# Kernel optimization log

Measured on AMD Instinct MI355X. Metric: run time of the kernel, lower is better.

Reference implementation:

```python
import jax, jax.numpy as jnp
import numpy as np

E = 16      # num_experts
K = 4       # num_experts_per_tok
H = 2048    # hidden_size
I = 1408    # moe_intermediate_size
SI = 5632   # shared expert intermediate size
CAP = 1024
NORM_TOPK = False


def setup_inputs() -> dict:
    key = jax.random.key(0)
    ks = jax.random.split(key, 9)
    def w(k, shape, fan_in):
        return jax.random.normal(k, shape, jnp.float32) * (fan_in ** -0.5)
    return {
        "hidden_states": jax.random.normal(ks[0], (1, 2048, H), jnp.float32),
        "gate_w":  w(ks[1], (E, H), H),        # router: Linear(H -> E), no bias
        "we_gate": w(ks[2], (E, I, H), H),     # per-expert gate_proj weights
        "we_up":   w(ks[3], (E, I, H), H),     # per-expert up_proj weights
        "we_down": w(ks[4], (E, H, I), I),     # per-expert down_proj weights
        "ws_gate": w(ks[5], (SI, H), H),       # shared expert gate_proj
        "ws_up":   w(ks[6], (SI, H), H),       # shared expert up_proj
        "ws_down": w(ks[7], (H, SI), SI),      # shared expert down_proj
        "sg_w":    w(ks[8], (1, H), H),        # shared_expert_gate: Linear(H -> 1)
    }


def reference(hidden_states, gate_w, we_gate, we_up, we_down,
              ws_gate, ws_up, ws_down, sg_w):
    B, S, Hd = hidden_states.shape
    x = hidden_states.reshape(-1, Hd)                      # [T, H]
    T = x.shape[0]

    # --- router ---
    router_logits = x @ gate_w.T                           # [T, E]
    probs = jax.nn.softmax(router_logits.astype(jnp.float32), axis=-1)
    topw, topi = jax.lax.top_k(probs, K)                   # [T, K]
    if NORM_TOPK:
        topw = topw / topw.sum(axis=-1, keepdims=True)

    # --- dispatch: flatten (token, slot) assignments ---
    A = T * K
    fe = topi.reshape(A)                                   # expert id per assignment
    fw = topw.reshape(A)                                   # routing weight per assignment
    ft = jnp.repeat(jnp.arange(T), K)                      # token id per assignment
    # position of each assignment within its expert (rank in arrival order)
    oh = jax.nn.one_hot(fe, E, dtype=jnp.int32)            # [A, E]
    pos = jnp.take_along_axis(jnp.cumsum(oh, axis=0) - 1, fe[:, None], axis=1)[:, 0]
    valid = pos < CAP
    # scatter tokens into per-expert buffers; overflow goes to dummy row CAP
    buf = jnp.zeros((E, CAP + 1, Hd), x.dtype)
    buf = buf.at[fe, jnp.where(valid, pos, CAP)].set(x[ft])[:, :CAP]  # [E, C, H]

    # --- per-expert SiLU-gated MLP (batched grouped GEMMs) ---
    g = jnp.einsum('ech,eih->eci', buf, we_gate)
    u = jnp.einsum('ech,eih->eci', buf, we_up)
    eo = jnp.einsum('eci,ehi->ech', jax.nn.silu(g) * u, we_down)      # [E, C, H]

    # --- combine: weighted scatter-add back to tokens ---
    ga = eo[fe, jnp.minimum(pos, CAP - 1)]                 # [A, H]
    wcomb = (fw * valid.astype(fw.dtype)).astype(x.dtype)
    y = jnp.zeros((T, Hd), x.dtype).at[ft].add(ga * wcomb[:, None])

    # --- shared expert with sigmoid gate ---
    sh = (jax.nn.silu(x @ ws_gate.T) * (x @ ws_up.T)) @ ws_down.T
    sh = jax.nn.sigmoid(x @ sg_w.T) * sh

    out = (y + sh).reshape(B, S, Hd)
    return out, router_logits
```

## Files before the change

### kernel.cpp

```cpp
#include <hip/hip_runtime.h>

#define T_TOK 2048
#define NE 16
#define KTOP 4
#define HD 2048
#define ID 1408
#define SID 5632
#define CAPACITY 1024

typedef __attribute__((ext_vector_type(8))) short short8;
typedef __attribute__((ext_vector_type(4))) float floatx4;

__device__ __forceinline__ short f2b(float f){
  union { float f; unsigned u; } v; v.f = f;
  unsigned r = v.u + 0x7fffu + ((v.u >> 16) & 1u);
  return (short)(r >> 16);
}
__device__ __forceinline__ float b2f(short s){
  union { float f; unsigned u; } v; v.u = ((unsigned)(unsigned short)s) << 16;
  return v.f;
}
__device__ __forceinline__ void gl16(const void* g, void* l){
  __builtin_amdgcn_global_load_lds(
      (const __attribute__((address_space(1))) void*)g,
      (__attribute__((address_space(3))) void*)l, 16, 0, 0);
}

__global__ void moe_zero(int* __restrict__ counts){
  if (threadIdx.x < NE) counts[threadIdx.x] = 0;
}

__global__ void moe_convert_all(const float* __restrict__ eg, const float* __restrict__ eu,
                                const float* __restrict__ ed, const float* __restrict__ sgp,
                                const float* __restrict__ sup, const float* __restrict__ sdp,
                                short* __restrict__ dst)
{
  const long long EW = (long long)NE * ID * HD / 8;
  const long long SW = (long long)SID * HD / 8;
  const long long total = 3 * EW + 3 * SW;
  long long stride = (long long)gridDim.x * blockDim.x;
  for (long long i = (long long)blockIdx.x * blockDim.x + threadIdx.x; i < total; i += stride){
    const float* s; long long j;
    if (i < 2 * EW){
      if (i < EW){ s = eg; j = i; } else { s = eu; j = i - EW; }
    } else if (i < 3 * EW){ s = ed; j = i - 2 * EW; }
    else if (i < 3 * EW + SW){ s = sgp; j = i - 3 * EW; }
    else if (i < 3 * EW + 2 * SW){ s = sup; j = i - 3 * EW - SW; }
    else { s = sdp; j = i - 3 * EW - 2 * SW; }
    float4 f0 = ((const float4*)s)[j * 2];
    float4 f1 = ((const float4*)s)[j * 2 + 1];
    short8 v = { f2b(f0.x), f2b(f0.y), f2b(f0.z), f2b(f0.w),
                 f2b(f1.x), f2b(f1.y), f2b(f1.z), f2b(f1.w) };
    ((short8*)dst)[i] = v;
  }
}

__global__ void moe_router(const float* __restrict__ x,
                           const float* __restrict__ gate_w,
                           const float* __restrict__ sg_w,
                           float* __restrict__ logits_out,
                           short* __restrict__ xb,
                           int* __restrict__ counts,
                           int* __restrict__ slot_token,
                           float* __restrict__ slot_w,
                           int* __restrict__ tslot,
                           float* __restrict__ tw,
                           float* __restrict__ sg)
{
  int wave = threadIdx.x >> 6, lane = threadIdx.x & 63;
  int t = (blockIdx.x << 2) + wave;
  if (t >= T_TOK) return;
  const float4* xr = (const float4*)(x + (size_t)t * HD);
  short8* xbw = (short8*)(xb + (size_t)t * HD);
  float acc[17];
  #pragma unroll
  for (int e = 0; e < 17; ++e) acc[e] = 0.f;
  #pragma unroll
  for (int j = 0; j < 4; ++j){
    int i4 = (j * 64 + lane) * 2;
    float4 x0 = xr[i4], x1 = xr[i4 + 1];
    short8 v = { f2b(x0.x), f2b(x0.y), f2b(x0.z), f2b(x0.w),
                 f2b(x1.x), f2b(x1.y), f2b(x1.z), f2b(x1.w) };
    xbw[j * 64 + lane] = v;
    #pragma unroll
    for (int e = 0; e < 16; ++e){
      const float4* gr = (const float4*)(gate_w + e * HD);
      float4 g0 = gr[i4], g1 = gr[i4 + 1];
      acc[e] += x0.x*g0.x + x0.y*g0.y + x0.z*g0.z + x0.w*g0.w
              + x1.x*g1.x + x1.y*g1.y + x1.z*g1.z + x1.w*g1.w;
    }
    const float4* sr = (const float4*)sg_w;
    float4 s0 = sr[i4], s1 = sr[i4 + 1];
    acc[16] += x0.x*s0.x + x0.y*s0.y + x0.z*s0.z + x0.w*s0.w
             + x1.x*s1.x + x1.y*s1.y + x1.z*s1.z + x1.w*s1.w;
  }
  #pragma unroll
  for (int e = 0; e < 17; ++e){
    float v = acc[e];
    #pragma unroll
    for (int off = 32; off > 0; off >>= 1) v += __shfl_xor(v, off, 64);
    acc[e] = v;
  }
  if (lane == 0){
    float m = acc[0];
    #pragma unroll
    for (int e = 1; e < 16; ++e) m = fmaxf(m, acc[e]);
    float p[16]; float s = 0.f;
    #pragma unroll
    for (int e = 0; e < 16; ++e){ p[e] = expf(acc[e] - m); s += p[e]; }
    float inv = 1.f / s;
    #pragma unroll
    for (int e = 0; e < 16; ++e) logits_out[t * 16 + e] = acc[e];
    unsigned used = 0;
    for (int k = 0; k < KTOP; ++k){
      float best = -1.f; int bi = 0;
      #pragma unroll
      for (int e = 0; e < 16; ++e){
        float pe = ((used >> e) & 1u) ? -1.f : p[e];
        if (pe > best){ best = pe; bi = e; }
      }
      used |= (1u << bi);
      int pos = atomicAdd(&counts[bi], 1);
      int enc = -1;
      if (pos < CAPACITY){
        slot_token[bi * CAPACITY + pos] = t;
        slot_w[bi * CAPACITY + pos] = best * inv;
        enc = bi * CAPACITY + pos;
      }
      tslot[t * KTOP + k] = enc;
      tw[t * KTOP + k] = best * inv;
    }
    sg[t] = 1.f / (1.f + expf(-acc[16]));
  }
}


template<int BF16W>
__global__ __launch_bounds__(256) void moe_gateup(
    const short* __restrict__ Asrc,
    const void* __restrict__ Wg_, const void* __restrict__ Wu_,
    short* __restrict__ Out,
    const int* __restrict__ counts, const int* __restrict__ slot_token,
    int Ndim, int Kdim, int expert_mode, int mtiles, int ntiles)
{
  int nwg = gridDim.x;
  int wg = ((blockIdx.x & 7) * (nwg >> 3)) + (blockIdx.x >> 3);
  int m_t = wg % mtiles; wg /= mtiles;
  int n_t = wg % ntiles; int e = wg / ntiles;

  int cnt = T_TOK; size_t woff = 0; short* out = Out;
  if (expert_mode){
    cnt = counts[e]; if (cnt > CAPACITY) cnt = CAPACITY;
    if (m_t * 128 >= cnt) return;
    woff = (size_t)e * Ndim * Kdim;
    out = Out + (size_t)e * CAPACITY * Ndim;
  }
  const int m0 = m_t * 128, n0 = n_t * 64;

  __shared__ __align__(16) char smem[2][32768];

  const int tid = threadIdx.x;
  const int lane = tid & 63, wave = tid >> 6;
  const int wr = wave >> 1, wc = wave & 1;
  const int lrow = lane & 15, lk = lane >> 4;

  const int srow = tid >> 3, pslot = tid & 7;
  const int lslot = pslot ^ (srow & 7);

  const short* aptr[4];
  #pragma unroll
  for (int i = 0; i < 4; ++i){
    int p = m0 + i * 32 + srow;
    const short* base;
    if (expert_mode){
      int q = (p < cnt) ? p : 0;
      base = Asrc + (size_t)slot_token[e * CAPACITY + q] * Kdim;
    } else base = Asrc + (size_t)p * Kdim;
    aptr[i] = base + (lslot << 3);
  }
  const short *bgp[2], *bup[2];
  const float *bgf[2], *buf2[2];
  #pragma unroll
  for (int i = 0; i < 2; ++i){
    size_t roff = (size_t)(n0 + i * 32 + srow) * Kdim + (lslot << 3);
    if (BF16W){
      bgp[i] = (const short*)Wg_ + woff + roff;
      bup[i] = (const short*)Wu_ + woff + roff;
    } else {
      bgf[i]  = (const float*)Wg_ + woff + roff;
      buf2[i] = (const float*)Wu_ + woff + roff;
    }
  }

  const floatx4 vzero = {0.f, 0.f, 0.f, 0.f};
  floatx4 accg[4][2], accu[4][2];
  #pragma unroll
  for (int i = 0; i < 4; ++i)
    #pragma unroll
    for (int j = 0; j < 2; ++j){ accg[i][j] = vzero; accu[i][j] = vzero; }

  const int fxor = lrow & 7;
  const int arowb = (wr * 64 + lrow) << 7;
  const int browb = (wc * 32 + lrow) << 7;

  if (BF16W){
    {
      char* b = smem[0];
      #pragma unroll
      for (int i = 0; i < 4; ++i) gl16(aptr[i], b + i * 4096 + tid * 16);
      #pragma unroll
      for (int i = 0; i < 2; ++i) gl16(bgp[i], b + 16384 + i * 4096 + tid * 16);
      #pragma unroll
      for (int i = 0; i < 2; ++i) gl16(bup[i], b + 24576 + i * 4096 + tid * 16);
    }
    __syncthreads();
    int cur = 0;
    for (int k0 = 0; k0 < Kdim; k0 += 64){
      if (k0 + 64 < Kdim){
        char* b = smem[cur ^ 1];
        #pragma unroll
        for (int i = 0; i < 4; ++i) gl16(aptr[i] + k0 + 64, b + i * 4096 + tid * 16);
        #pragma unroll
        for (int i = 0; i < 2; ++i) gl16(bgp[i] + k0 + 64, b + 16384 + i * 4096 + tid * 16);
        #pragma unroll
        for (int i = 0; i < 2; ++i) gl16(bup[i] + k0 + 64, b + 24576 + i * 4096 + tid * 16);
      }
      const char* bb = smem[cur];
      #pragma unroll
      for (int kh = 0; kh < 2; ++kh){
        const int soff = (((kh << 2) | lk) ^ fxor) << 4;
        short8 a[4], bg[2], bu[2];
        #pragma unroll
        for (int mf = 0; mf < 4; ++mf)
          a[mf] = *(const short8*)(bb + arowb + (mf << 11) + soff);
        #pragma unroll
        for (int nf = 0; nf < 2; ++nf){
          bg[nf] = *(const short8*)(bb + 16384 + browb + (nf << 11) + soff);
          bu[nf] = *(const short8*)(bb + 24576 + browb + (nf << 11) + soff);
        }
        #pragma unroll
        for (int mf = 0; mf < 4; ++mf)
          #pragma unroll
          for (int nf = 0; nf < 2; ++nf){
            accg[mf][nf] = __builtin_amdgcn_mfma_f32_16x16x32_bf16(a[mf], bg[nf], accg[mf][nf], 0, 0, 0);
            accu[mf][nf] = __builtin_amdgcn_mfma_f32_16x16x32_bf16(a[mf], bu[nf], accu[mf][nf], 0, 0, 0);
          }
      }
      __syncthreads();
      cur ^= 1;
    }
  } else {
    char* sA = smem[0]; char* sBg = sA + 16384; char* sBu = sA + 24576;
    for (int k0 = 0; k0 < Kdim; k0 += 64){
      __syncthreads();
      #pragma unroll
      for (int i = 0; i < 4; ++i){
        short8 v = *(const short8*)(aptr[i] + k0);
        *(short8*)(sA + i * 4096 + tid * 16) = v;
      }
      #pragma unroll
      for (int i = 0; i < 2; ++i){
        float4 f0 = *(const float4*)(bgf[i] + k0);
        float4 f1 = *(const float4*)(bgf[i] + k0 + 4);
        short8 v = { f2b(f0.x), f2b(f0.y), f2b(f0.z), f2b(f0.w),
                     f2b(f1.x), f2b(f1.y), f2b(f1.z), f2b(f1.w) };
        *(short8*)(sBg + i * 4096 + tid * 16) = v;
        float4 g0 = *(const float4*)(buf2[i] + k0);
        float4 g1 = *(const float4*)(buf2[i] + k0 + 4);
        short8 w = { f2b(g0.x), f2b(g0.y), f2b(g0.z), f2b(g0.w),
                     f2b(g1.x), f2b(g1.y), f2b(g1.z), f2b(g1.w) };
        *(short8*)(sBu + i * 4096 + tid * 16) = w;
      }
      __syncthreads();
      #pragma unroll
      for (int kh = 0; kh < 2; ++kh){
        const int soff = (((kh << 2) | lk) ^ fxor) << 4;
        short8 a[4], bg[2], bu[2];
        #pragma unroll
        for (int mf = 0; mf < 4; ++mf)
          a[mf] = *(const short8*)(sA + arowb + (mf << 11) + soff);
        #pragma unroll
        for (int nf = 0; nf < 2; ++nf){
          bg[nf] = *(const short8*)(sBg + browb + (nf << 11) + soff);
          bu[nf] = *(const short8*)(sBu + browb + (nf << 11) + soff);
        }
        #pragma unroll
        for (int mf = 0; mf < 4; ++mf)
          #pragma unroll
          for (int nf = 0; nf < 2; ++nf){
            accg[mf][nf] = __builtin_amdgcn_mfma_f32_16x16x32_bf16(a[mf], bg[nf], accg[mf][nf], 0, 0, 0);
            accu[mf][nf] = __builtin_amdgcn_mfma_f32_16x16x32_bf16(a[mf], bu[nf], accu[mf][nf], 0, 0, 0);
          }
      }
    }
  }

  const int colbase = n0 + wc * 32 + lrow;
  #pragma unroll
  for (int mf = 0; mf < 4; ++mf){
    int pr = m0 + wr * 64 + mf * 16 + lk * 4;
    #pragma unroll
    for (int nf = 0; nf < 2; ++nf){
      floatx4 g4 = accg[mf][nf], u4 = accu[mf][nf];
      int col = colbase + nf * 16;
      #pragma unroll
      for (int r = 0; r < 4; ++r){
        float gv = g4[r], uv = u4[r];
        float a = (gv / (1.f + __expf(-gv))) * uv;
        out[(size_t)(pr + r) * Ndim + col] = f2b(a);
      }
    }
  }
}

template<int BF16W, int NF>
__global__ __launch_bounds__(256) void moe_down(
    const short* __restrict__ Asrc, const void* __restrict__ Wd_,
    float* __restrict__ y, short* __restrict__ eo,
    const int* __restrict__ counts, const int* __restrict__ slot_token,
    const float* __restrict__ slot_w, const float* __restrict__ sgate,
    int Kdim, int expert_mode, int mtiles, int ntiles)
{
  constexpr int BN = NF * 32;
  int nwg = gridDim.x;
  int wg = ((blockIdx.x & 7) * (nwg >> 3)) + (blockIdx.x >> 3);
  int m_t = wg % mtiles; wg /= mtiles;
  int n_t = wg % ntiles; int e = wg / ntiles;

  int cnt = T_TOK; const short* ab = Asrc; size_t woff = 0;
  if (expert_mode){
    cnt = counts[e]; if (cnt > CAPACITY) cnt = CAPACITY;
    if (m_t * 128 >= cnt) return;
    ab = Asrc + (size_t)e * CAPACITY * Kdim;
    woff = (size_t)e * HD * Kdim;
  }
  const int m0 = m_t * 128, n0 = n_t * BN;

  __shared__ __align__(16) char smem[2][16384 + NF * 4096];

  const int tid = threadIdx.x;
  const int lane = tid & 63, wave = tid >> 6;
  const int wr = wave >> 1, wc = wave & 1;
  const int lrow = lane & 15, lk = lane >> 4;

  const int srow = tid >> 3, pslot = tid & 7;
  const int lslot = pslot ^ (srow & 7);

  const short* aptr[4];
  #pragma unroll
  for (int i = 0; i < 4; ++i)
    aptr[i] = ab + (size_t)(m0 + i * 32 + srow) * Kdim + (lslot << 3);
  const short* bbp[NF];
  const float* bbf[NF];
  #pragma unroll
  for (int i = 0; i < NF; ++i){
    size_t roff = (size_t)(n0 + i * 32 + srow) * Kdim + (lslot << 3);
    if (BF16W) bbp[i] = (const short*)Wd_ + woff + roff;
    else       bbf[i] = (const float*)Wd_ + woff + roff;
  }

  const floatx4 vzero = {0.f, 0.f, 0.f, 0.f};
  floatx4 acc[4][NF];
  #pragma unroll
  for (int i = 0; i < 4; ++i)
    #pragma unroll
    for (int j = 0; j < NF; ++j) acc[i][j] = vzero;

  const int fxor = lrow & 7;
  const int arowb = (wr * 64 + lrow) << 7;
  const int browb = (wc * (NF * 16) + lrow) << 7;

  if (BF16W){
    {
      char* b = smem[0];
      #pragma unroll
      for (int i = 0; i < 4; ++i) gl16(aptr[i], b + i * 4096 + tid * 16);
      #pragma unroll
      for (int i = 0; i < NF; ++i) gl16(bbp[i], b + 16384 + i * 4096 + tid * 16);
    }
    __syncthreads();
    int cur = 0;
    for (int k0 = 0; k0 < Kdim; k0 += 64){
      if (k0 + 64 < Kdim){
        char* b = smem[cur ^ 1];
        #pragma unroll
        for (int i = 0; i < 4; ++i) gl16(aptr[i] + k0 + 64, b + i * 4096 + tid * 16);
        #pragma unroll
        for (int i = 0; i < NF; ++i) gl16(bbp[i] + k0 + 64, b + 16384 + i * 4096 + tid * 16);
      }
      const char* bb = smem[cur];
      #pragma unroll
      for (int kh = 0; kh < 2; ++kh){
        const int soff = (((kh << 2) | lk) ^ fxor) << 4;
        short8 a[4], b[NF];
        #pragma unroll
        for (int mf = 0; mf < 4; ++mf)
          a[mf] = *(const short8*)(bb + arowb + (mf << 11) + soff);
        #pragma unroll
        for (int nf = 0; nf < NF; ++nf)
          b[nf] = *(const short8*)(bb + 16384 + browb + (nf << 11) + soff);
        #pragma unroll
        for (int mf = 0; mf < 4; ++mf)
          #pragma unroll
          for (int nf = 0; nf < NF; ++nf)
            acc[mf][nf] = __builtin_amdgcn_mfma_f32_16x16x32_bf16(a[mf], b[nf], acc[mf][nf], 0, 0, 0);
      }
      __syncthreads();
      cur ^= 1;
    }
  } else {
    char* sA = smem[0]; char* sB = sA + 16384;
    for (int k0 = 0; k0 < Kdim; k0 += 64){
      __syncthreads();
      #pragma unroll
      for (int i = 0; i < 4; ++i){
        short8 v = *(const short8*)(aptr[i] + k0);
        *(short8*)(sA + i * 4096 + tid * 16) = v;
      }
      #pragma unroll
      for (int i = 0; i < NF; ++i){
        float4 f0 = *(const float4*)(bbf[i] + k0);
        float4 f1 = *(const float4*)(bbf[i] + k0 + 4);
        short8 w = { f2b(f0.x), f2b(f0.y), f2b(f0.z), f2b(f0.w),
                     f2b(f1.x), f2b(f1.y), f2b(f1.z), f2b(f1.w) };
        *(short8*)(sB + i * 4096 + tid * 16) = w;
      }
      __syncthreads();
      #pragma unroll
      for (int kh = 0; kh < 2; ++kh){
        const int soff = (((kh << 2) | lk) ^ fxor) << 4;
        short8 a[4], b[NF];
        #pragma unroll
        for (int mf = 0; mf < 4; ++mf)
          a[mf] = *(const short8*)(sA + arowb + (mf << 11) + soff);
        #pragma unroll
        for (int nf = 0; nf < NF; ++nf)
          b[nf] = *(const short8*)(sB + browb + (nf << 11) + soff);
        #pragma unroll
        for (int mf = 0; mf < 4; ++mf)
          #pragma unroll
          for (int nf = 0; nf < NF; ++nf)
            acc[mf][nf] = __builtin_amdgcn_mfma_f32_16x16x32_bf16(a[mf], b[nf], acc[mf][nf], 0, 0, 0);
      }
    }
  }

  const int colb = n0 + wc * (NF * 16) + lrow;
  if (expert_mode){
    if (eo){
      #pragma unroll
      for (int mf = 0; mf < 4; ++mf){
        int pr = m0 + wr * 64 + mf * 16 + lk * 4;
        #pragma unroll
        for (int r = 0; r < 4; ++r){
          int p = pr + r;
          #pragma unroll
          for (int nf = 0; nf < NF; ++nf)
            eo[(size_t)(e * CAPACITY + p) * HD + colb + nf * 16] = f2b(acc[mf][nf][r]);
        }
      }
    } else {
      #pragma unroll
      for (int mf = 0; mf < 4; ++mf){
        int pr = m0 + wr * 64 + mf * 16 + lk * 4;
        #pragma unroll
        for (int r = 0; r < 4; ++r){
          int p = pr + r;
          if (p < cnt){
            int tok = slot_token[e * CAPACITY + p];
            float w = slot_w[e * CAPACITY + p];
            #pragma unroll
            for (int nf = 0; nf < NF; ++nf)
              atomicAdd(&y[(size_t)tok * HD + colb + nf * 16], w * acc[mf][nf][r]);
          }
        }
      }
    }
  } else {
    #pragma unroll
    for (int mf = 0; mf < 4; ++mf){
      int pr = m0 + wr * 64 + mf * 16 + lk * 4;
      #pragma unroll
      for (int r = 0; r < 4; ++r){
        int t = pr + r;
        float sv = sgate[t];
        #pragma unroll
        for (int nf = 0; nf < NF; ++nf)
          y[(size_t)t * HD + colb + nf * 16] = sv * acc[mf][nf][r];
      }
    }
  }
}

__global__ void moe_combine(const short* __restrict__ eo,
                            const int* __restrict__ tslot,
                            const float* __restrict__ tw,
                            float* __restrict__ y)
{
  int t = blockIdx.x;
  int o = threadIdx.x << 3;
  float* yp = y + (size_t)t * HD + o;
  float4 a0 = *(const float4*)yp, a1 = *(const float4*)(yp + 4);
  float acc[8] = {a0.x, a0.y, a0.z, a0.w, a1.x, a1.y, a1.z, a1.w};
  #pragma unroll
  for (int k = 0; k < KTOP; ++k){
    int s = tslot[t * KTOP + k];
    if (s >= 0){
      float w = tw[t * KTOP + k];
      short8 v = *(const short8*)(eo + (size_t)s * HD + o);
      #pragma unroll
      for (int j = 0; j < 8; ++j) acc[j] += w * b2f(v[j]);
    }
  }
  float4 r0 = {acc[0], acc[1], acc[2], acc[3]};
  float4 r1 = {acc[4], acc[5], acc[6], acc[7]};
  *(float4*)yp = r0; *(float4*)(yp + 4) = r1;
}

extern "C" void kernel_launch(void* const* d_in, const int* in_sizes, int n_in,
                              void* d_out, int out_size, void* d_ws, size_t ws_size,
                              hipStream_t stream)
{
  (void)in_sizes; (void)n_in; (void)out_size;
  const float* x       = (const float*)d_in[0];
  const float* gate_w  = (const float*)d_in[1];
  const float* we_gate = (const float*)d_in[2];
  const float* we_up   = (const float*)d_in[3];
  const float* we_down = (const float*)d_in[4];
  const float* wsg     = (const float*)d_in[5];
  const float* wsu     = (const float*)d_in[6];
  const float* wsd     = (const float*)d_in[7];
  const float* sg_w    = (const float*)d_in[8];

  float* y      = (float*)d_out;
  float* logits = y + (size_t)T_TOK * HD;

  const size_t SZ_XB  = (size_t)T_TOK * HD * 2;
  const size_t SZ_WE  = (size_t)NE * ID * HD * 2;
  const size_t SZ_WS  = (size_t)SID * HD * 2;
  const size_t SZ_ACT = (size_t)NE * CAPACITY * ID * 2;
  const size_t SZ_ACS = (size_t)T_TOK * SID * 2;
  const size_t SZ_EO  = (size_t)NE * CAPACITY * HD * 2;
  const size_t SZ_SMALL = 65536 + 65536 + 32768 + 32768 + 256 + 8192;

  const size_t NEED_B = SZ_XB + 3 * SZ_WE + 3 * SZ_WS + SZ_ACT + SZ_ACS + SZ_SMALL;
  const size_t NEED_A = NEED_B + SZ_EO;

  char* ws = (char*)d_ws;
  size_t off = 0;
  short* xb   = (short*)(ws + off); off += SZ_XB;
  short* wbeg = (short*)(ws + off); off += SZ_WE;
  short* wbeu = (short*)(ws + off); off += SZ_WE;
  short* wbed = (short*)(ws + off); off += SZ_WE;
  short* wbsg = (short*)(ws + off); off += SZ_WS;
  short* wbsu = (short*)(ws + off); off += SZ_WS;
  short* wbsd = (short*)(ws + off); off += SZ_WS;
  short* act  = (short*)(ws + off); off += SZ_ACT;
  short* acts = (short*)(ws + off); off += SZ_ACS;
  short* eo   = (short*)(ws + off);
  if (ws_size >= NEED_A) off += SZ_EO; else eo = nullptr;
  int*   slot_token = (int*)  (ws + off); off += 65536;
  float* slot_w     = (float*)(ws + off); off += 65536;
  int*   tslot      = (int*)  (ws + off); off += 32768;
  float* tw         = (float*)(ws + off); off += 32768;
  int*   counts     = (int*)  (ws + off); off += 256;
  float* sg         = (float*)(ws + off);

  if (ws_size >= NEED_B){
    moe_zero<<<1, 64, 0, stream>>>(counts);
    moe_convert_all<<<2048, 256, 0, stream>>>(we_gate, we_up, we_down, wsg, wsu, wsd, wbeg);
    moe_router<<<512, 256, 0, stream>>>(x, gate_w, sg_w, logits, xb,
                                        counts, slot_token, slot_w, tslot, tw, sg);
    moe_gateup<1><<<16 * 88, 256, 0, stream>>>(xb, wbsg, wbsu, acts,
                                               nullptr, nullptr, SID, HD, 0, 16, 88);
    moe_gateup<1><<<8 * 22 * NE, 256, 0, stream>>>(xb, wbeg, wbeu, act,
                                                   counts, slot_token, ID, HD, 1, 8, 22);
    moe_down<1, 2><<<16 * 32, 256, 0, stream>>>(acts, wbsd, y, nullptr, nullptr, nullptr,
                                                nullptr, sg, SID, 0, 16, 32);
    moe_down<1, 4><<<8 * 16 * NE, 256, 0, stream>>>(act, wbed, y, eo, counts, slot_token,
                                                    slot_w, nullptr, ID, 1, 8, 16);
    if (eo) moe_combine<<<T_TOK, 256, 0, stream>>>(eo, tslot, tw, y);
  } else {
    size_t o2 = 0;
    short* xb2   = (short*)(ws + o2); o2 += SZ_XB;
    short* act2  = (short*)(ws + o2); o2 += SZ_ACT;
    short* acts2 = (short*)(ws + o2); o2 += SZ_ACS;
    int*   st2 = (int*)  (ws + o2); o2 += 65536;
    float* sw2 = (float*)(ws + o2); o2 += 65536;
    int*   ts2 = (int*)  (ws + o2); o2 += 32768;
    float* tw2 = (float*)(ws + o2); o2 += 32768;
    int*   cn2 = (int*)  (ws + o2); o2 += 256;
    float* sg2 = (float*)(ws + o2);
    moe_zero<<<1, 64, 0, stream>>>(cn2);
    moe_router<<<512, 256, 0, stream>>>(x, gate_w, sg_w, logits, xb2,
                                        cn2, st2, sw2, ts2, tw2, sg2);
    moe_gateup<0><<<16 * 88, 256, 0, stream>>>(xb2, wsg, wsu, acts2,
                                               nullptr, nullptr, SID, HD, 0, 16, 88);
    moe_gateup<0><<<8 * 22 * NE, 256, 0, stream>>>(xb2, we_gate, we_up, act2,
                                                   cn2, st2, ID, HD, 1, 8, 22);
    moe_down<0, 2><<<16 * 32, 256, 0, stream>>>(acts2, wsd, y, nullptr, nullptr, nullptr,
                                                nullptr, sg2, SID, 0, 16, 32);
    moe_down<0, 4><<<8 * 16 * NE, 256, 0, stream>>>(act2, we_down, y, nullptr, cn2, st2,
                                                    sw2, nullptr, ID, 1, 8, 16);
  }
}
```

Before: 841.6 us.

## Fuse fp32-to-bf16 weight conversion into GEMM loaders and drop pre-convert pass

Removes the separate kernel that converted all expert and shared weights to bf16 every call. The grouped GEMMs now read fp32 weights directly into registers, convert them with packed v_cvt_pk_bf16_f32, and write them to the next LDS buffer while the MFMAs consume the current one. The activation tiles keep their async global-to-LDS prefetch. This avoids writing and rereading a full bf16 copy of the weights, but each GEMM now streams twice the weight bytes and spends extra VALU work and registers on conversion. It also changes rounding for tie and NaN cases through the hardware convert instruction.

```diff
diff --git a/kernel.cpp b/kernel.cpp
--- a/kernel.cpp
+++ b/kernel.cpp
@@ -20,6 +20,17 @@
   union { float f; unsigned u; } v; v.u = ((unsigned)(unsigned short)s) << 16;
   return v.f;
 }
+__device__ __forceinline__ unsigned cvt_pk(float a, float b){
+  unsigned r;
+  asm("v_cvt_pk_bf16_f32 %0, %1, %2" : "=v"(r) : "v"(a), "v"(b));
+  return r;
+}
+__device__ __forceinline__ short8 cvt8(float4 a, float4 b){
+  union { unsigned d[4]; short8 s; } u;
+  u.d[0] = cvt_pk(a.x, a.y); u.d[1] = cvt_pk(a.z, a.w);
+  u.d[2] = cvt_pk(b.x, b.y); u.d[3] = cvt_pk(b.z, b.w);
+  return u.s;
+}
 __device__ __forceinline__ void gl16(const void* g, void* l){
   __builtin_amdgcn_global_load_lds(
       (const __attribute__((address_space(1))) void*)g,
@@ -28,31 +39,6 @@
 
 __global__ void moe_zero(int* __restrict__ counts){
   if (threadIdx.x < NE) counts[threadIdx.x] = 0;
-}
-
-__global__ void moe_convert_all(const float* __restrict__ eg, const float* __restrict__ eu,
-                                const float* __restrict__ ed, const float* __restrict__ sgp,
-                                const float* __restrict__ sup, const float* __restrict__ sdp,
-                                short* __restrict__ dst)
-{
-  const long long EW = (long long)NE * ID * HD / 8;
-  const long long SW = (long long)SID * HD / 8;
-  const long long total = 3 * EW + 3 * SW;
-  long long stride = (long long)gridDim.x * blockDim.x;
-  for (long long i = (long long)blockIdx.x * blockDim.x + threadIdx.x; i < total; i += stride){
-    const float* s; long long j;
-    if (i < 2 * EW){
-      if (i < EW){ s = eg; j = i; } else { s = eu; j = i - EW; }
-    } else if (i < 3 * EW){ s = ed; j = i - 2 * EW; }
-    else if (i < 3 * EW + SW){ s = sgp; j = i - 3 * EW; }
-    else if (i < 3 * EW + 2 * SW){ s = sup; j = i - 3 * EW - SW; }
-    else { s = sdp; j = i - 3 * EW - 2 * SW; }
-    float4 f0 = ((const float4*)s)[j * 2];
-    float4 f1 = ((const float4*)s)[j * 2 + 1];
-    short8 v = { f2b(f0.x), f2b(f0.y), f2b(f0.z), f2b(f0.w),
-                 f2b(f1.x), f2b(f1.y), f2b(f1.z), f2b(f1.w) };
-    ((short8*)dst)[i] = v;
-  }
 }
 
 __global__ void moe_router(const float* __restrict__ x,
@@ -79,9 +65,7 @@
   for (int j = 0; j < 4; ++j){
     int i4 = (j * 64 + lane) * 2;
     float4 x0 = xr[i4], x1 = xr[i4 + 1];
-    short8 v = { f2b(x0.x), f2b(x0.y), f2b(x0.z), f2b(x0.w),
-                 f2b(x1.x), f2b(x1.y), f2b(x1.z), f2b(x1.w) };
-    xbw[j * 64 + lane] = v;
+    xbw[j * 64 + lane] = cvt8(x0, x1);
     #pragma unroll
     for (int e = 0; e < 16; ++e){
       const float4* gr = (const float4*)(gate_w + e * HD);
@@ -135,10 +119,9 @@
 }
 
 
-template<int BF16W>
 __global__ __launch_bounds__(256) void moe_gateup(
     const short* __restrict__ Asrc,
-    const void* __restrict__ Wg_, const void* __restrict__ Wu_,
+    const float* __restrict__ Wg_, const float* __restrict__ Wu_,
     short* __restrict__ Out,
     const int* __restrict__ counts, const int* __restrict__ slot_token,
     int Ndim, int Kdim, int expert_mode, int mtiles, int ntiles)
@@ -178,18 +161,12 @@
     } else base = Asrc + (size_t)p * Kdim;
     aptr[i] = base + (lslot << 3);
   }
-  const short *bgp[2], *bup[2];
-  const float *bgf[2], *buf2[2];
+  const float *bsrc[4];
   #pragma unroll
   for (int i = 0; i < 2; ++i){
     size_t roff = (size_t)(n0 + i * 32 + srow) * Kdim + (lslot << 3);
-    if (BF16W){
-      bgp[i] = (const short*)Wg_ + woff + roff;
-      bup[i] = (const short*)Wu_ + woff + roff;
-    } else {
-      bgf[i]  = (const float*)Wg_ + woff + roff;
-      buf2[i] = (const float*)Wu_ + woff + roff;
-    }
+    bsrc[i]     = Wg_ + woff + roff;
+    bsrc[i + 2] = Wu_ + woff + roff;
   }
 
   const floatx4 vzero = {0.f, 0.f, 0.f, 0.f};
@@ -202,97 +179,61 @@
   const int fxor = lrow & 7;
   const int arowb = (wr * 64 + lrow) << 7;
   const int browb = (wc * 32 + lrow) << 7;
-
-  if (BF16W){
-    {
-      char* b = smem[0];
-      #pragma unroll
-      for (int i = 0; i < 4; ++i) gl16(aptr[i], b + i * 4096 + tid * 16);
-      #pragma unroll
-      for (int i = 0; i < 2; ++i) gl16(bgp[i], b + 16384 + i * 4096 + tid * 16);
-      #pragma unroll
-      for (int i = 0; i < 2; ++i) gl16(bup[i], b + 24576 + i * 4096 + tid * 16);
-    }
-    __syncthreads();
-    int cur = 0;
-    for (int k0 = 0; k0 < Kdim; k0 += 64){
-      if (k0 + 64 < Kdim){
-        char* b = smem[cur ^ 1];
-        #pragma unroll
-        for (int i = 0; i < 4; ++i) gl16(aptr[i] + k0 + 64, b + i * 4096 + tid * 16);
-        #pragma unroll
-        for (int i = 0; i < 2; ++i) gl16(bgp[i] + k0 + 64, b + 16384 + i * 4096 + tid * 16);
-        #pragma unroll
-        for (int i = 0; i < 2; ++i) gl16(bup[i] + k0 + 64, b + 24576 + i * 4096 + tid * 16);
-      }
-      const char* bb = smem[cur];
-      #pragma unroll
-      for (int kh = 0; kh < 2; ++kh){
-        const int soff = (((kh << 2) | lk) ^ fxor) << 4;
-        short8 a[4], bg[2], bu[2];
-        #pragma unroll
-        for (int mf = 0; mf < 4; ++mf)
-          a[mf] = *(const short8*)(bb + arowb + (mf << 11) + soff);
+  const int bwoff = 16384 + (tid << 4);
+
+  float4 breg[4][2];
+  #pragma unroll
+  for (int i = 0; i < 4; ++i) gl16(aptr[i], smem[0] + i * 4096 + tid * 16);
+  #pragma unroll
+  for (int i = 0; i < 4; ++i){
+    breg[i][0] = *(const float4*)(bsrc[i]);
+    breg[i][1] = *(const float4*)(bsrc[i] + 4);
+  }
+  #pragma unroll
+  for (int i = 0; i < 4; ++i)
+    *(short8*)(smem[0] + bwoff + i * 4096) = cvt8(breg[i][0], breg[i][1]);
+  __syncthreads();
+
+  int cur = 0;
+  for (int k0 = 0; k0 < Kdim; k0 += 64){
+    const bool more = (k0 + 64) < Kdim;
+    if (more){
+      #pragma unroll
+      for (int i = 0; i < 4; ++i) gl16(aptr[i] + k0 + 64, smem[cur ^ 1] + i * 4096 + tid * 16);
+      #pragma unroll
+      for (int i = 0; i < 4; ++i){
+        breg[i][0] = *(const float4*)(bsrc[i] + k0 + 64);
+        breg[i][1] = *(const float4*)(bsrc[i] + k0 + 68);
+      }
+    }
+    const char* bb = smem[cur];
+    #pragma unroll
+    for (int kh = 0; kh < 2; ++kh){
+      const int soff = (((kh << 2) | lk) ^ fxor) << 4;
+      short8 a[4], bg[2], bu[2];
+      #pragma unroll
+      for (int mf = 0; mf < 4; ++mf)
+        a[mf] = *(const short8*)(bb + arowb + (mf << 11) + soff);
+      #pragma unroll
+      for (int nf = 0; nf < 2; ++nf){
+        bg[nf] = *(const short8*)(bb + 16384 + browb + (nf << 11) + soff);
+        bu[nf] = *(const short8*)(bb + 24576 + browb + (nf << 11) + soff);
+      }
+      #pragma unroll
+      for (int mf = 0; mf < 4; ++mf)
         #pragma unroll
         for (int nf = 0; nf < 2; ++nf){
-          bg[nf] = *(const short8*)(bb + 16384 + browb + (nf << 11) + soff);
-          bu[nf] = *(const short8*)(bb + 24576 + browb + (nf << 11) + soff);
+          accg[mf][nf] = __builtin_amdgcn_mfma_f32_16x16x32_bf16(a[mf], bg[nf], accg[mf][nf], 0, 0, 0);
+          accu[mf][nf] = __builtin_amdgcn_mfma_f32_16x16x32_bf16(a[mf], bu[nf], accu[mf][nf], 0, 0, 0);
         }
-        #pragma unroll
-        for (int mf = 0; mf < 4; ++mf)
-          #pragma unroll
-          for (int nf = 0; nf < 2; ++nf){
-            accg[mf][nf] = __builtin_amdgcn_mfma_f32_16x16x32_bf16(a[mf], bg[nf], accg[mf][nf], 0, 0, 0);
-            accu[mf][nf] = __builtin_amdgcn_mfma_f32_16x16x32_bf16(a[mf], bu[nf], accu[mf][nf], 0, 0, 0);
-          }
-      }
-      __syncthreads();
-      cur ^= 1;
-    }
-  } else {
-    char* sA = smem[0]; char* sBg = sA + 16384; char* sBu = sA + 24576;
-    for (int k0 = 0; k0 < Kdim; k0 += 64){
-      __syncthreads();
-      #pragma unroll
-      for (int i = 0; i < 4; ++i){
-        short8 v = *(const short8*)(aptr[i] + k0);
-        *(short8*)(sA + i * 4096 + tid * 16) = v;
-      }
-      #pragma unroll
-      for (int i = 0; i < 2; ++i){
-        float4 f0 = *(const float4*)(bgf[i] + k0);
-        float4 f1 = *(const float4*)(bgf[i] + k0 + 4);
-        short8 v = { f2b(f0.x), f2b(f0.y), f2b(f0.z), f2b(f0.w),
-                     f2b(f1.x), f2b(f1.y), f2b(f1.z), f2b(f1.w) };
-        *(short8*)(sBg + i * 4096 + tid * 16) = v;
-        float4 g0 = *(const float4*)(buf2[i] + k0);
-        float4 g1 = *(const float4*)(buf2[i] + k0 + 4);
-        short8 w = { f2b(g0.x), f2b(g0.y), f2b(g0.z), f2b(g0.w),
-                     f2b(g1.x), f2b(g1.y), f2b(g1.z), f2b(g1.w) };
-        *(short8*)(sBu + i * 4096 + tid * 16) = w;
-      }
-      __syncthreads();
-      #pragma unroll
-      for (int kh = 0; kh < 2; ++kh){
-        const int soff = (((kh << 2) | lk) ^ fxor) << 4;
-        short8 a[4], bg[2], bu[2];
-        #pragma unroll
-        for (int mf = 0; mf < 4; ++mf)
-          a[mf] = *(const short8*)(sA + arowb + (mf << 11) + soff);
-        #pragma unroll
-        for (int nf = 0; nf < 2; ++nf){
-          bg[nf] = *(const short8*)(sBg + browb + (nf << 11) + soff);
-          bu[nf] = *(const short8*)(sBu + browb + (nf << 11) + soff);
-        }
-        #pragma unroll
-        for (int mf = 0; mf < 4; ++mf)
-          #pragma unroll
-          for (int nf = 0; nf < 2; ++nf){
-            accg[mf][nf] = __builtin_amdgcn_mfma_f32_16x16x32_bf16(a[mf], bg[nf], accg[mf][nf], 0, 0, 0);
-            accu[mf][nf] = __builtin_amdgcn_mfma_f32_16x16x32_bf16(a[mf], bu[nf], accu[mf][nf], 0, 0, 0);
-          }
-      }
-    }
+    }
+    if (more){
+      #pragma unroll
+      for (int i = 0; i < 4; ++i)
+        *(short8*)(smem[cur ^ 1] + bwoff + i * 4096) = cvt8(breg[i][0], breg[i][1]);
+    }
+    __syncthreads();
+    cur ^= 1;
   }
 
   const int colbase = n0 + wc * 32 + lrow;
@@ -313,9 +254,9 @@
   }
 }
 
-template<int BF16W, int NF>
+template<int NF>
 __global__ __launch_bounds__(256) void moe_down(
-    const short* __restrict__ Asrc, const void* __restrict__ Wd_,
+    const short* __restrict__ Asrc, const float* __restrict__ Wd_,
     float* __restrict__ y, short* __restrict__ eo,
     const int* __restrict__ counts, const int* __restrict__ slot_token,
     const float* __restrict__ slot_w, const float* __restrict__ sgate,
@@ -350,14 +291,10 @@
   #pragma unroll
   for (int i = 0; i < 4; ++i)
     aptr[i] = ab + (size_t)(m0 + i * 32 + srow) * Kdim + (lslot << 3);
-  const short* bbp[NF];
-  const float* bbf[NF];
-  #pragma unroll
-  for (int i = 0; i < NF; ++i){
-    size_t roff = (size_t)(n0 + i * 32 + srow) * Kdim + (lslot << 3);
-    if (BF16W) bbp[i] = (const short*)Wd_ + woff + roff;
-    else       bbf[i] = (const float*)Wd_ + woff + roff;
-  }
+  const float* bsrc[NF];
+  #pragma unroll
+  for (int i = 0; i < NF; ++i)
+    bsrc[i] = Wd_ + woff + (size_t)(n0 + i * 32 + srow) * Kdim + (lslot << 3);
 
   const floatx4 vzero = {0.f, 0.f, 0.f, 0.f};
   floatx4 acc[4][NF];
@@ -369,80 +306,57 @@
   const int fxor = lrow & 7;
   const int arowb = (wr * 64 + lrow) << 7;
   const int browb = (wc * (NF * 16) + lrow) << 7;
-
-  if (BF16W){
-    {
-      char* b = smem[0];
-      #pragma unroll
-      for (int i = 0; i < 4; ++i) gl16(aptr[i], b + i * 4096 + tid * 16);
-      #pragma unroll
-      for (int i = 0; i < NF; ++i) gl16(bbp[i], b + 16384 + i * 4096 + tid * 16);
-    }
-    __syncthreads();
-    int cur = 0;
-    for (int k0 = 0; k0 < Kdim; k0 += 64){
-      if (k0 + 64 < Kdim){
-        char* b = smem[cur ^ 1];
-        #pragma unroll
-        for (int i = 0; i < 4; ++i) gl16(aptr[i] + k0 + 64, b + i * 4096 + tid * 16);
-        #pragma unroll
-        for (int i = 0; i < NF; ++i) gl16(bbp[i] + k0 + 64, b + 16384 + i * 4096 + tid * 16);
-      }
-      const char* bb = smem[cur];
-      #pragma unroll
-      for (int kh = 0; kh < 2; ++kh){
-        const int soff = (((kh << 2) | lk) ^ fxor) << 4;
-        short8 a[4], b[NF];
-        #pragma unroll
-        for (int mf = 0; mf < 4; ++mf)
-          a[mf] = *(const short8*)(bb + arowb + (mf << 11) + soff);
+  const int bwoff = 16384 + (tid << 4);
+
+  float4 breg[NF][2];
+  #pragma unroll
+  for (int i = 0; i < 4; ++i) gl16(aptr[i], smem[0] + i * 4096 + tid * 16);
+  #pragma unroll
+  for (int i = 0; i < NF; ++i){
+    breg[i][0] = *(const float4*)(bsrc[i]);
+    breg[i][1] = *(const float4*)(bsrc[i] + 4);
+  }
+  #pragma unroll
+  for (int i = 0; i < NF; ++i)
+    *(short8*)(smem[0] + bwoff + i * 4096) = cvt8(breg[i][0], breg[i][1]);
+  __syncthreads();
+
+  int cur = 0;
+  for (int k0 = 0; k0 < Kdim; k0 += 64){
+    const bool more = (k0 + 64) < Kdim;
+    if (more){
+      #pragma unroll
+      for (int i = 0; i < 4; ++i) gl16(aptr[i] + k0 + 64, smem[cur ^ 1] + i * 4096 + tid * 16);
+      #pragma unroll
+      for (int i = 0; i < NF; ++i){
+        breg[i][0] = *(const float4*)(bsrc[i] + k0 + 64);
+        breg[i][1] = *(const float4*)(bsrc[i] + k0 + 68);
+      }
+    }
+    const char* bb = smem[cur];
+    #pragma unroll
+    for (int kh = 0; kh < 2; ++kh){
+      const int soff = (((kh << 2) | lk) ^ fxor) << 4;
+      short8 a[4], b[NF];
+      #pragma unroll
+      for (int mf = 0; mf < 4; ++mf)
+        a[mf] = *(const short8*)(bb + arowb + (mf << 11) + soff);
+      #pragma unroll
+      for (int nf = 0; nf < NF; ++nf)
+        b[nf] = *(const short8*)(bb + 16384 + browb + (nf << 11) + soff);
+      #pragma unroll
+      for (int mf = 0; mf < 4; ++mf)
         #pragma unroll
         for (int nf = 0; nf < NF; ++nf)
-          b[nf] = *(const short8*)(bb + 16384 + browb + (nf << 11) + soff);
-        #pragma unroll
-        for (int mf = 0; mf < 4; ++mf)
-          #pragma unroll
-          for (int nf = 0; nf < NF; ++nf)
-            acc[mf][nf] = __builtin_amdgcn_mfma_f32_16x16x32_bf16(a[mf], b[nf], acc[mf][nf], 0, 0, 0);
-      }
-      __syncthreads();
-      cur ^= 1;
-    }
-  } else {
-    char* sA = smem[0]; char* sB = sA + 16384;
-    for (int k0 = 0; k0 < Kdim; k0 += 64){
-      __syncthreads();
-      #pragma unroll
-      for (int i = 0; i < 4; ++i){
-        short8 v = *(const short8*)(aptr[i] + k0);
-        *(short8*)(sA + i * 4096 + tid * 16) = v;
-      }
-      #pragma unroll
-      for (int i = 0; i < NF; ++i){
-        float4 f0 = *(const float4*)(bbf[i] + k0);
-        float4 f1 = *(const float4*)(bbf[i] + k0 + 4);
-        short8 w = { f2b(f0.x), f2b(f0.y), f2b(f0.z), f2b(f0.w),
-                     f2b(f1.x), f2b(f1.y), f2b(f1.z), f2b(f1.w) };
-        *(short8*)(sB + i * 4096 + tid * 16) = w;
-      }
-      __syncthreads();
-      #pragma unroll
-      for (int kh = 0; kh < 2; ++kh){
-        const int soff = (((kh << 2) | lk) ^ fxor) << 4;
-        short8 a[4], b[NF];
-        #pragma unroll
-        for (int mf = 0; mf < 4; ++mf)
-          a[mf] = *(const short8*)(sA + arowb + (mf << 11) + soff);
-        #pragma unroll
-        for (int nf = 0; nf < NF; ++nf)
-          b[nf] = *(const short8*)(sB + browb + (nf << 11) + soff);
-        #pragma unroll
-        for (int mf = 0; mf < 4; ++mf)
-          #pragma unroll
-          for (int nf = 0; nf < NF; ++nf)
-            acc[mf][nf] = __builtin_amdgcn_mfma_f32_16x16x32_bf16(a[mf], b[nf], acc[mf][nf], 0, 0, 0);
-      }
-    }
+          acc[mf][nf] = __builtin_amdgcn_mfma_f32_16x16x32_bf16(a[mf], b[nf], acc[mf][nf], 0, 0, 0);
+    }
+    if (more){
+      #pragma unroll
+      for (int i = 0; i < NF; ++i)
+        *(short8*)(smem[cur ^ 1] + bwoff + i * 4096) = cvt8(breg[i][0], breg[i][1]);
+    }
+    __syncthreads();
+    cur ^= 1;
   }
 
   const int colb = n0 + wc * (NF * 16) + lrow;
@@ -536,25 +450,17 @@
   float* logits = y + (size_t)T_TOK * HD;
 
   const size_t SZ_XB  = (size_t)T_TOK * HD * 2;
-  const size_t SZ_WE  = (size_t)NE * ID * HD * 2;
-  const size_t SZ_WS  = (size_t)SID * HD * 2;
   const size_t SZ_ACT = (size_t)NE * CAPACITY * ID * 2;
   const size_t SZ_ACS = (size_t)T_TOK * SID * 2;
   const size_t SZ_EO  = (size_t)NE * CAPACITY * HD * 2;
   const size_t SZ_SMALL = 65536 + 65536 + 32768 + 32768 + 256 + 8192;
 
-  const size_t NEED_B = SZ_XB + 3 * SZ_WE + 3 * SZ_WS + SZ_ACT + SZ_ACS + SZ_SMALL;
+  const size_t NEED_B = SZ_XB + SZ_ACT + SZ_ACS + SZ_SMALL;
   const size_t NEED_A = NEED_B + SZ_EO;
 
   char* ws = (char*)d_ws;
   size_t off = 0;
   short* xb   = (short*)(ws + off); off += SZ_XB;
-  short* wbeg = (short*)(ws + off); off += SZ_WE;
-  short* wbeu = (short*)(ws + off); off += SZ_WE;
-  short* wbed = (short*)(ws + off); off += SZ_WE;
-  short* wbsg = (short*)(ws + off); off += SZ_WS;
-  short* wbsu = (short*)(ws + off); off += SZ_WS;
-  short* wbsd = (short*)(ws + off); off += SZ_WS;
   short* act  = (short*)(ws + off); off += SZ_ACT;
   short* acts = (short*)(ws + off); off += SZ_ACS;
   short* eo   = (short*)(ws + off);
@@ -566,41 +472,16 @@
   int*   counts     = (int*)  (ws + off); off += 256;
   float* sg         = (float*)(ws + off);
 
-  if (ws_size >= NEED_B){
-    moe_zero<<<1, 64, 0, stream>>>(counts);
-    moe_convert_all<<<2048, 256, 0, stream>>>(we_gate, we_up, we_down, wsg, wsu, wsd, wbeg);
-    moe_router<<<512, 256, 0, stream>>>(x, gate_w, sg_w, logits, xb,
-                                        counts, slot_token, slot_w, tslot, tw, sg);
-    moe_gateup<1><<<16 * 88, 256, 0, stream>>>(xb, wbsg, wbsu, acts,
-                                               nullptr, nullptr, SID, HD, 0, 16, 88);
-    moe_gateup<1><<<8 * 22 * NE, 256, 0, stream>>>(xb, wbeg, wbeu, act,
-                                                   counts, slot_token, ID, HD, 1, 8, 22);
-    moe_down<1, 2><<<16 * 32, 256, 0, stream>>>(acts, wbsd, y, nullptr, nullptr, nullptr,
-                                                nullptr, sg, SID, 0, 16, 32);
-    moe_down<1, 4><<<8 * 16 * NE, 256, 0, stream>>>(act, wbed, y, eo, counts, slot_token,
-                                                    slot_w, nullptr, ID, 1, 8, 16);
-    if (eo) moe_combine<<<T_TOK, 256, 0, stream>>>(eo, tslot, tw, y);
-  } else {
-    size_t o2 = 0;
-    short* xb2   = (short*)(ws + o2); o2 += SZ_XB;
-    short* act2  = (short*)(ws + o2); o2 += SZ_ACT;
-    short* acts2 = (short*)(ws + o2); o2 += SZ_ACS;
-    int*   st2 = (int*)  (ws + o2); o2 += 65536;
-    float* sw2 = (float*)(ws + o2); o2 += 65536;
-    int*   ts2 = (int*)  (ws + o2); o2 += 32768;
-    float* tw2 = (float*)(ws + o2); o2 += 32768;
-    int*   cn2 = (int*)  (ws + o2); o2 += 256;
-    float* sg2 = (float*)(ws + o2);
-    moe_zero<<<1, 64, 0, stream>>>(cn2);
-    moe_router<<<512, 256, 0, stream>>>(x, gate_w, sg_w, logits, xb2,
-                                        cn2, st2, sw2, ts2, tw2, sg2);
-    moe_gateup<0><<<16 * 88, 256, 0, stream>>>(xb2, wsg, wsu, acts2,
-                                               nullptr, nullptr, SID, HD, 0, 16, 88);
-    moe_gateup<0><<<8 * 22 * NE, 256, 0, stream>>>(xb2, we_gate, we_up, act2,
-                                                   cn2, st2, ID, HD, 1, 8, 22);
-    moe_down<0, 2><<<16 * 32, 256, 0, stream>>>(acts2, wsd, y, nullptr, nullptr, nullptr,
-                                                nullptr, sg2, SID, 0, 16, 32);
-    moe_down<0, 4><<<8 * 16 * NE, 256, 0, stream>>>(act2, we_down, y, nullptr, cn2, st2,
-                                                    sw2, nullptr, ID, 1, 8, 16);
-  }
-}
+  moe_zero<<<1, 64, 0, stream>>>(counts);
+  moe_router<<<512, 256, 0, stream>>>(x, gate_w, sg_w, logits, xb,
+                                      counts, slot_token, slot_w, tslot, tw, sg);
+  moe_gateup<<<16 * 88, 256, 0, stream>>>(xb, wsg, wsu, acts,
+                                          nullptr, nullptr, SID, HD, 0, 16, 88);
+  moe_gateup<<<8 * 22 * NE, 256, 0, stream>>>(xb, we_gate, we_up, act,
+                                              counts, slot_token, ID, HD, 1, 8, 22);
+  moe_down<2><<<16 * 32, 256, 0, stream>>>(acts, wsd, y, nullptr, nullptr, nullptr,
+                                           nullptr, sg, SID, 0, 16, 32);
+  moe_down<4><<<8 * 16 * NE, 256, 0, stream>>>(act, we_down, y, eo, counts, slot_token,
+                                               slot_w, nullptr, ID, 1, 8, 16);
+  if (eo) moe_combine<<<T_TOK, 256, 0, stream>>>(eo, tslot, tw, y);
+}
```

Measured after the change: 800.4 us. -4.9%, faster.
